# Optimization experiments

Hardware: AMD Instinct MI355X
Metric: run time of the kernel (lower is better)

## Reference

```python
import jax, jax.numpy as jnp
import numpy as np

B, T, C, H = 8, 1024, 768, 12
HD = C // H  # 64

def setup_inputs() -> dict:
    key = jax.random.key(0)
    ks = jax.random.split(key, 5)
    s = 0.02
    return {
        "x": jax.random.normal(ks[0], (B, T, C), dtype=jnp.float32),
        "w_attn": jax.random.normal(ks[1], (C, 3 * C), dtype=jnp.float32) * s,
        "b_attn": jnp.zeros((3 * C,), dtype=jnp.float32),
        "w_proj": jax.random.normal(ks[2], (C, C), dtype=jnp.float32) * s,
        "b_proj": jnp.zeros((C,), dtype=jnp.float32),
    }

def reference(x, w_attn, b_attn, w_proj, b_proj):
    Bx, Tx, Cx = x.shape
    qkv = x @ w_attn + b_attn                      # [B,T,3C]
    q, k, v = jnp.split(qkv, 3, axis=-1)
    # [B,H,T,hd]
    q = q.reshape(Bx, Tx, H, HD).transpose(0, 2, 1, 3)
    k = k.reshape(Bx, Tx, H, HD).transpose(0, 2, 1, 3)
    v = v.reshape(Bx, Tx, H, HD).transpose(0, 2, 1, 3)
    scale = 1.0 / jnp.sqrt(jnp.asarray(HD, dtype=x.dtype))
    scores = jnp.einsum('bhqd,bhkd->bhqk', q, k) * scale  # [B,H,T,T]
    causal = jnp.tril(jnp.ones((Tx, Tx), dtype=bool))
    scores = jnp.where(causal, scores, jnp.asarray(-jnp.inf, dtype=x.dtype))
    weights = jax.nn.softmax(scores, axis=-1)
    y = jnp.einsum('bhqk,bhkd->bhqd', weights, v)  # [B,H,T,hd]
    y = y.transpose(0, 2, 1, 3).reshape(Bx, Tx, Cx)
    return y @ w_proj + b_proj
```

## Files before the change

### kernel.cpp

```cpp
#include <hip/hip_runtime.h>
#include <cstdint>
#include <cstddef>

#define B_  8
#define T_  1024
#define C_  768
#define H_  12
#define HD_ 64
#define K3_ 2304

typedef unsigned short u16;
typedef __attribute__((ext_vector_type(8))) short bf16x8;
typedef __attribute__((ext_vector_type(4))) float f32x4;

#define MFMA __builtin_amdgcn_mfma_f32_16x16x32_bf16

__device__ __forceinline__ u16 f2bf(float f) {
    unsigned u = __builtin_bit_cast(unsigned, f);
    u += 0x7fffu + ((u >> 16) & 1u);
    return (u16)(u >> 16);
}

__device__ __forceinline__ unsigned pk2bf(float a, float b) {
    unsigned ua = __builtin_bit_cast(unsigned, a) + 0x8000u;
    unsigned ub = __builtin_bit_cast(unsigned, b) + 0x8000u;
    return (ua >> 16) | (ub & 0xffff0000u);
}

#define GLL16(gp, lp) __builtin_amdgcn_global_load_lds( \
    (__attribute__((address_space(1))) unsigned int*)(gp), \
    (__attribute__((address_space(3))) unsigned int*)(lp), 16, 0, 0)

__device__ __forceinline__ void tcvt_tile(const float* __restrict__ in, u16* __restrict__ out,
                                          int R, int Cc, int bx, int by, int tid, float* tile ) {
    int bc = bx * 32, br = by * 32;
    int tx = tid & 31, ty = tid >> 5;
    #pragma unroll
    for (int kk = 0; kk < 32; kk += 8)
        tile[(ty + kk) * 33 + tx] = in[(size_t)(br + ty + kk) * Cc + bc + tx];
    __syncthreads();
    #pragma unroll
    for (int kk = 0; kk < 32; kk += 8)
        out[(size_t)(bc + ty + kk) * R + br + tx] = f2bf(tile[tx * 33 + ty + kk]);
}

__global__ void prep(const float* __restrict__ x, u16* __restrict__ xb,
                     const float* __restrict__ wa, u16* __restrict__ wat,
                     const float* __restrict__ wp, u16* __restrict__ wpt) {
    __shared__ float tile[32 * 33];
    int bid = blockIdx.x, tid = threadIdx.x;
    if (bid < 6144) {
        int i = bid * 256 + tid;
        float4 v = ((const float4*)x)[i];
        ushort4 o;
        o.x = f2bf(v.x); o.y = f2bf(v.y); o.z = f2bf(v.z); o.w = f2bf(v.w);
        ((ushort4*)xb)[i] = o;
    } else if (bid < 6144 + 1728) {
        int b = bid - 6144;
        tcvt_tile(wa, wat, C_, K3_, b % 72, b / 72, tid, tile);
    } else {
        int b = bid - 7872;
        tcvt_tile(wp, wpt, C_, C_, b % 24, b / 24, tid, tile);
    }
}

#define VMW5 asm volatile("s_waitcnt vmcnt(5)" ::: "memory")
#define VMW0 asm volatile("s_waitcnt vmcnt(0)" ::: "memory")
#define BAR  __builtin_amdgcn_s_barrier()

__device__ __forceinline__ void gemm_pipe(const u16* __restrict__ A, const u16* __restrict__ Bt,
                                          int m0, int n0, u16* SM, f32x4 (&acc)[4][3]) {
    const int K = C_;
    int tid = threadIdx.x;
    int lane = tid & 63, wv = tid >> 6;
    int wr = wv >> 2, wc = wv & 3;
    int r16 = lane & 15, quad = lane >> 4;
    int sw = r16 & 7;
    int x0 = (quad ^ sw) * 8;
    int x1 = ((4 + quad) ^ sw) * 8;
    int arow = (wr * 64 + r16) * 64;
    int brow = (wc * 48 + r16) * 64;
    int tr = tid >> 3;
    int tb = (tid & 7) ^ (tr & 7);
    const u16* Ag = A  + (size_t)(m0 + tr) * K + tb * 8;
    const u16* Bg = Bt + (size_t)(n0 + tr) * K + tb * 8;
    u16* SLa = SM + tid * 8;
    u16* SLb = SM + 24576 + tid * 8;
    const u16* SMB = SM + 24576;

#define STG_T(ss, kO) { \
    GLL16(Ag + (kO),                       SLa + (ss) * 8192); \
    GLL16(Ag + (size_t)64 * K + (kO),      SLa + (ss) * 8192 + 4096); \
    GLL16(Bg + (kO),                       SLb + (ss) * 12288); \
    GLL16(Bg + (size_t)64 * K + (kO),      SLb + (ss) * 12288 + 4096); \
    GLL16(Bg + (size_t)128 * K + (kO),     SLb + (ss) * 12288 + 8192); }
#define RDH(rs, XC, af, bf) { \
    const u16* Ar_ = SM  + (rs) * 8192  + arow; \
    const u16* Br_ = SMB + (rs) * 12288 + brow; \
    _Pragma("unroll") for (int i_ = 0; i_ < 4; i_++) af[i_] = *(const bf16x8*)&Ar_[i_ * 1024 + (XC)]; \
    _Pragma("unroll") for (int j_ = 0; j_ < 3; j_++) bf[j_] = *(const bf16x8*)&Br_[j_ * 1024 + (XC)]; }
#define MMH(af, bf) { \
    __builtin_amdgcn_s_setprio(1); \
    _Pragma("unroll") for (int i_ = 0; i_ < 4; i_++) \
    _Pragma("unroll") for (int j_ = 0; j_ < 3; j_++) \
        acc[i_][j_] = MFMA(af[i_], bf[j_], acc[i_][j_], 0, 0, 0); \
    __builtin_amdgcn_s_setprio(0); }
#define PHASE(rs, ts, kO) { \
    bf16x8 a0[4], b0[3], a1[4], b1[3]; \
    RDH(rs, x0, a0, b0); RDH(rs, x1, a1, b1); \
    STG_T(ts, kO); \
    MMH(a0, b0); MMH(a1, b1); \
    VMW5; BAR; }

    STG_T(0, 0); STG_T(1, 64);
    VMW5; BAR;

    int kS = 128;
    #pragma unroll
    for (int o = 0; o < 3; ++o) {
        PHASE(0, 2, kS);
        PHASE(1, 0, kS + 64);
        PHASE(2, 1, kS + 128);
        kS += 192;
    }
    PHASE(0, 2, 704);
    {
        bf16x8 a0[4], b0[3], a1[4], b1[3];
        RDH(1, x0, a0, b0); RDH(1, x1, a1, b1);
        MMH(a0, b0); MMH(a1, b1);
        VMW0; BAR;
    }
    {
        bf16x8 a0[4], b0[3], a1[4], b1[3];
        RDH(2, x0, a0, b0); RDH(2, x1, a1, b1);
        MMH(a0, b0); MMH(a1, b1);
    }
#undef STG_T
#undef RDH
#undef MMH
#undef PHASE
}

__launch_bounds__(512)
__global__ void gemm_qkv(const u16* __restrict__ A, const u16* __restrict__ Bt,
                         const float* __restrict__ bias,
                         u16* __restrict__ q, u16* __restrict__ k, u16* __restrict__ v) {
    __shared__ __align__(16) u16 SM[61440];
    int id = blockIdx.x;
    int xcd = id & 7, j = id >> 3;
    int m0 = (xcd * 8 + (j & 7)) * 128;
    int np = j >> 3;
    f32x4 acc[4][3] = {};
    gemm_pipe(A, Bt, m0, np * 192, SM, acc);

    int tid = threadIdx.x;
    int lane = tid & 63, wv = tid >> 6;
    int wr = wv >> 2, wc = wv & 3;
    int r16 = lane & 15, quad = lane >> 4;
    __syncthreads();

    int sec = np >> 2;
    int cc0 = (np & 3) * 192;
    int b = m0 >> 10, t0 = m0 & 1023;

    if (sec == 2) {
        #pragma unroll
        for (int i = 0; i < 4; i++) {
            #pragma unroll
            for (int jj = 0; jj < 3; jj++) {
                int cc = cc0 + wc * 48 + jj * 16 + r16;
                float bv = bias[2 * C_ + cc];
                int h = cc >> 6, hd = cc & 63;
                int t = t0 + wr * 64 + i * 16 + quad * 4;
                ushort4 ov;
                ov.x = f2bf(acc[i][jj][0] + bv); ov.y = f2bf(acc[i][jj][1] + bv);
                ov.z = f2bf(acc[i][jj][2] + bv); ov.w = f2bf(acc[i][jj][3] + bv);
                *(ushort4*)(v + (((size_t)b * H_ + h) * HD_ + hd) * T_ + t) = ov;
            }
        }
    } else {
        float scale = (sec == 0) ? 0.125f : 1.0f;
        u16* dst = (sec == 0) ? q : k;
        u16 (*Cs)[200] = (u16(*)[200])SM;
        #pragma unroll
        for (int i = 0; i < 4; i++)
            #pragma unroll
            for (int jj = 0; jj < 3; jj++) {
                int col = wc * 48 + jj * 16 + r16;
                float bv = bias[sec * C_ + cc0 + col];
                #pragma unroll
                for (int r = 0; r < 4; r++)
                    Cs[wr * 64 + i * 16 + quad * 4 + r][col] = f2bf((acc[i][jj][r] + bv) * scale);
            }
        __syncthreads();
        int h0 = cc0 >> 6;
        int rsel = tid >> 3;
        int ch = tid & 7;
        #pragma unroll
        for (int p = 0; p < 2; p++)
            #pragma unroll
            for (int h3 = 0; h3 < 3; h3++) {
                int rl = p * 64 + rsel;
                uint4 val = *(const uint4*)&Cs[rl][h3 * 64 + ch * 8];
                *(uint4*)(dst + (((size_t)b * H_ + h0 + h3) * T_ + t0 + rl) * HD_ + ch * 8) = val;
            }
    }
}

__launch_bounds__(512)
__global__ void gemm_proj(const u16* __restrict__ A, const u16* __restrict__ Bt,
                          const float* __restrict__ bias, float* __restrict__ out) {
    __shared__ __align__(16) u16 SM[61440];
    int id = blockIdx.x;
    int xcd = id & 7, j = id >> 3;
    int m0 = (xcd * 8 + (j & 7)) * 128;
    int n0 = (j >> 3) * 192;
    f32x4 acc[4][3] = {};
    gemm_pipe(A, Bt, m0, n0, SM, acc);

    int tid = threadIdx.x;
    int lane = tid & 63, wv = tid >> 6;
    int wr = wv >> 2, wc = wv & 3;
    int r16 = lane & 15, quad = lane >> 4;
    #pragma unroll
    for (int i = 0; i < 4; i++) {
        #pragma unroll
        for (int jj = 0; jj < 3; jj++) {
            int gn = n0 + wc * 48 + jj * 16 + r16;
            float bv = bias[gn];
            #pragma unroll
            for (int r = 0; r < 4; r++) {
                int gm = m0 + wr * 64 + i * 16 + quad * 4 + r;
                out[(size_t)gm * C_ + gn] = acc[i][jj][r] + bv;
            }
        }
    }
}

__launch_bounds__(256, 2)
__global__ void attn(const u16* __restrict__ q, const u16* __restrict__ k,
                     const u16* __restrict__ v, u16* __restrict__ y) {
    __shared__ __align__(16) u16 Kb[2][64][64];
    __shared__ __align__(16) u16 Vb[2][64][64];
    __shared__ __align__(16) u16 P[4][2][16][72];
    int tid = threadIdx.x, lane = tid & 63, w = tid >> 6;
    int r16 = lane & 15, quad = lane >> 4;
    int id = blockIdx.x;
    int bh = id % 96;
    int bi = id / 96;
    int b = bh / H_, h = bh - b * H_;
    int x = bi * 4 + w;
    int t_lo = x, t_hi = 63 - x;
    int qb_lo = t_lo * 16, qb_hi = t_hi * 16;
    const u16* qh = q + (size_t)bh * T_ * HD_;
    const u16* kh = k + (size_t)bh * T_ * HD_;
    const u16* vh = v + (size_t)bh * HD_ * T_;

    bf16x8 ql0 = *(const bf16x8*)(qh + (size_t)(qb_lo + r16) * HD_ + quad * 8);
    bf16x8 ql1 = *(const bf16x8*)(qh + (size_t)(qb_lo + r16) * HD_ + 32 + quad * 8);
    bf16x8 qh0 = *(const bf16x8*)(qh + (size_t)(qb_hi + r16) * HD_ + quad * 8);
    bf16x8 qh1 = *(const bf16x8*)(qh + (size_t)(qb_hi + r16) * HD_ + 32 + quad * 8);

    f32x4 oL[4] = {}, oH[4] = {};
    float lL = 0.f, lH = 0.f;
    int qyL = qb_lo + r16, qyH = qb_hi + r16;
    int ilo_last = bi;
    int n64 = __builtin_amdgcn_readfirstlane(16 - bi);

    int srow = lane >> 3;
    int scb  = (lane & 7) ^ srow;
    const u16* kst = kh + (size_t)(w * 16 + srow) * HD_ + scb * 8;
    const u16* vst = vh + (size_t)(w * 16 + srow) * T_ + scb * 8;
    int swz = (r16 & 7);

    {
        #pragma unroll
        for (int s2 = 0; s2 < 2; s2++) {
            GLL16(kst + (size_t)(s2 * 8) * HD_, &Kb[0][w * 16 + s2 * 8][0] + lane * 8);
            GLL16(vst + (size_t)(s2 * 8) * T_,  &Vb[0][w * 16 + s2 * 8][0] + lane * 8);
        }
    }
    __syncthreads();

    for (int it = 0; it < n64; ++it) {
        int kv0 = it * 64;
        int buf = it & 1;
        bool lo_on = (it <= ilo_last);
        if (it + 1 < n64) {
            int kvn = kv0 + 64;
            #pragma unroll
            for (int s2 = 0; s2 < 2; s2++) {
                GLL16(kst + (size_t)(kvn + s2 * 8) * HD_, &Kb[buf ^ 1][w * 16 + s2 * 8][0] + lane * 8);
                GLL16(vst + (size_t)(s2 * 8) * T_ + kvn,  &Vb[buf ^ 1][w * 16 + s2 * 8][0] + lane * 8);
            }
        }
        bf16x8 kf[4][2];
        #pragma unroll
        for (int n = 0; n < 4; n++)
            #pragma unroll
            for (int c = 0; c < 2; c++)
                kf[n][c] = *(const bf16x8*)&Kb[buf][n * 16 + r16][((c * 4 + quad) ^ swz) * 8];
        f32x4 sH[4] = {};
        #pragma unroll
        for (int n = 0; n < 4; n++) {
            sH[n] = MFMA(kf[n][0], qh0, sH[n], 0, 0, 0);
            sH[n] = MFMA(kf[n][1], qh1, sH[n], 0, 0, 0);
        }
        if (it == n64 - 1) {
            #pragma unroll
            for (int n = 0; n < 4; n++)
                #pragma unroll
                for (int r = 0; r < 4; r++)
                    if (kv0 + n * 16 + quad * 4 + r > qyH) sH[n][r] = -1e30f;
        }
        #pragma unroll
        for (int n = 0; n < 4; n++) {
            float p0 = __expf(sH[n][0]);
            float p1 = __expf(sH[n][1]);
            float p2 = __expf(sH[n][2]);
            float p3 = __expf(sH[n][3]);
            lH += (p0 + p1) + (p2 + p3);
            uint2 pd; pd.x = pk2bf(p0, p1); pd.y = pk2bf(p2, p3);
            *(uint2*)&P[w][1][r16][n * 16 + quad * 4] = pd;
        }
        if (lo_on) {
            f32x4 sL[4] = {};
            #pragma unroll
            for (int n = 0; n < 4; n++) {
                sL[n] = MFMA(kf[n][0], ql0, sL[n], 0, 0, 0);
                sL[n] = MFMA(kf[n][1], ql1, sL[n], 0, 0, 0);
            }
            if (it == ilo_last) {
                #pragma unroll
                for (int n = 0; n < 4; n++)
                    #pragma unroll
                    for (int r = 0; r < 4; r++)
                        if (kv0 + n * 16 + quad * 4 + r > qyL) sL[n][r] = -1e30f;
            }
            #pragma unroll
            for (int n = 0; n < 4; n++) {
                float p0 = __expf(sL[n][0]);
                float p1 = __expf(sL[n][1]);
                float p2 = __expf(sL[n][2]);
                float p3 = __expf(sL[n][3]);
                lL += (p0 + p1) + (p2 + p3);
                uint2 pd; pd.x = pk2bf(p0, p1); pd.y = pk2bf(p2, p3);
                *(uint2*)&P[w][0][r16][n * 16 + quad * 4] = pd;
            }
        }
        bf16x8 vf[4][2];
        #pragma unroll
        for (int j = 0; j < 4; j++)
            #pragma unroll
            for (int c = 0; c < 2; c++)
                vf[j][c] = *(const bf16x8*)&Vb[buf][j * 16 + r16][((c * 4 + quad) ^ swz) * 8];
        #pragma unroll
        for (int c = 0; c < 2; c++) {
            bf16x8 pfH = *(const bf16x8*)&P[w][1][r16][c * 32 + quad * 8];
            #pragma unroll
            for (int j = 0; j < 4; j++)
                oH[j] = MFMA(vf[j][c], pfH, oH[j], 0, 0, 0);
        }
        if (lo_on) {
            #pragma unroll
            for (int c = 0; c < 2; c++) {
                bf16x8 pfL = *(const bf16x8*)&P[w][0][r16][c * 32 + quad * 8];
                #pragma unroll
                for (int j = 0; j < 4; j++)
                    oL[j] = MFMA(vf[j][c], pfL, oL[j], 0, 0, 0);
            }
        }
        __syncthreads();
    }

    lH += __shfl_xor(lH, 16, 64);
    lH += __shfl_xor(lH, 32, 64);
    lL += __shfl_xor(lL, 16, 64);
    lL += __shfl_xor(lL, 32, 64);
    float invH = 1.f / lH, invL = 1.f / lL;
    int tqH = qb_hi + r16, tqL = qb_lo + r16;
    #pragma unroll
    for (int j = 0; j < 4; j++) {
        ushort4 ovH, ovL;
        ovH.x = f2bf(oH[j][0] * invH); ovH.y = f2bf(oH[j][1] * invH);
        ovH.z = f2bf(oH[j][2] * invH); ovH.w = f2bf(oH[j][3] * invH);
        ovL.x = f2bf(oL[j][0] * invL); ovL.y = f2bf(oL[j][1] * invL);
        ovL.z = f2bf(oL[j][2] * invL); ovL.w = f2bf(oL[j][3] * invL);
        *(ushort4*)(y + ((size_t)b * T_ + tqH) * C_ + h * 64 + j * 16 + quad * 4) = ovH;
        *(ushort4*)(y + ((size_t)b * T_ + tqL) * C_ + h * 64 + j * 16 + quad * 4) = ovL;
    }
}

extern "C" void kernel_launch(void* const* d_in, const int* in_sizes, int n_in,
                              void* d_out, int out_size, void* d_ws, size_t ws_size,
                              hipStream_t stream) {
    const float* x      = (const float*)d_in[0];
    const float* w_attn = (const float*)d_in[1];
    const float* b_attn = (const float*)d_in[2];
    const float* w_proj = (const float*)d_in[3];
    const float* b_proj = (const float*)d_in[4];
    float* out = (float*)d_out;

    char* ws = (char*)d_ws;
    size_t off = 0;
    auto alloc = [&](size_t bytes) {
        void* p = ws + off;
        off += (bytes + 255) & ~(size_t)255;
        return p;
    };
    const size_t M = (size_t)B_ * T_;
    u16* x_bf = (u16*)alloc(M * C_ * 2);
    u16* wat  = (u16*)alloc((size_t)K3_ * C_ * 2);
    u16* wpt  = (u16*)alloc((size_t)C_ * C_ * 2);
    u16* qb   = (u16*)alloc((size_t)B_ * H_ * T_ * HD_ * 2);
    u16* kb   = (u16*)alloc((size_t)B_ * H_ * T_ * HD_ * 2);
    u16* vb   = (u16*)alloc((size_t)B_ * H_ * T_ * HD_ * 2);
    u16* yb   = (u16*)alloc(M * C_ * 2);

    prep<<<6144 + 1728 + 576, 256, 0, stream>>>(x, x_bf, w_attn, wat, w_proj, wpt);
    gemm_qkv<<<768, 512, 0, stream>>>(x_bf, wat, b_attn, qb, kb, vb);
    attn<<<8 * 96, 256, 0, stream>>>(qb, kb, vb, yb);
    gemm_proj<<<256, 512, 0, stream>>>(yb, wpt, b_proj, out);
}
```

Baseline: 159.2 us.

## Shrink GEMM tiles to 128x96 with 4 waves and double-buffered LDS

Both projection GEMMs change from 512-thread blocks computing 128x192 tiles with a triple-buffered LDS pipeline to 256-thread blocks computing 128x96 tiles with a double-buffered pipeline, which halves LDS use and allows two blocks per CU. The goal is more resident blocks and better load balance across CUs (twice as many blocks). The trade-off is a shallower prefetch with two barriers per k-step and more redundant A-tile loads across the N blocks. The q/k epilogue writes are remapped to match the narrower tile.

Result: no change. 159.1 us (-0.1%).

```diff
diff --git a/kernel.cpp b/kernel.cpp
--- a/kernel.cpp
+++ b/kernel.cpp
@@ -64,7 +64,7 @@
     }
 }
 
-#define VMW5 asm volatile("s_waitcnt vmcnt(5)" ::: "memory")
+#define VMW7 asm volatile("s_waitcnt vmcnt(7)" ::: "memory")
 #define VMW0 asm volatile("s_waitcnt vmcnt(0)" ::: "memory")
 #define BAR  __builtin_amdgcn_s_barrier()
 
@@ -73,7 +73,7 @@
     const int K = C_;
     int tid = threadIdx.x;
     int lane = tid & 63, wv = tid >> 6;
-    int wr = wv >> 2, wc = wv & 3;
+    int wr = wv >> 1, wc = wv & 1;
     int r16 = lane & 15, quad = lane >> 4;
     int sw = r16 & 7;
     int x0 = (quad ^ sw) * 8;
@@ -85,18 +85,20 @@
     const u16* Ag = A  + (size_t)(m0 + tr) * K + tb * 8;
     const u16* Bg = Bt + (size_t)(n0 + tr) * K + tb * 8;
     u16* SLa = SM + tid * 8;
-    u16* SLb = SM + 24576 + tid * 8;
-    const u16* SMB = SM + 24576;
+    u16* SLb = SM + 16384 + tid * 8;
+    const u16* SMB = SM + 16384;
 
 #define STG_T(ss, kO) { \
     GLL16(Ag + (kO),                       SLa + (ss) * 8192); \
+    GLL16(Ag + (size_t)32 * K + (kO),      SLa + (ss) * 8192 + 2048); \
     GLL16(Ag + (size_t)64 * K + (kO),      SLa + (ss) * 8192 + 4096); \
-    GLL16(Bg + (kO),                       SLb + (ss) * 12288); \
-    GLL16(Bg + (size_t)64 * K + (kO),      SLb + (ss) * 12288 + 4096); \
-    GLL16(Bg + (size_t)128 * K + (kO),     SLb + (ss) * 12288 + 8192); }
+    GLL16(Ag + (size_t)96 * K + (kO),      SLa + (ss) * 8192 + 6144); \
+    GLL16(Bg + (kO),                       SLb + (ss) * 6144); \
+    GLL16(Bg + (size_t)32 * K + (kO),      SLb + (ss) * 6144 + 2048); \
+    GLL16(Bg + (size_t)64 * K + (kO),      SLb + (ss) * 6144 + 4096); }
 #define RDH(rs, XC, af, bf) { \
-    const u16* Ar_ = SM  + (rs) * 8192  + arow; \
-    const u16* Br_ = SMB + (rs) * 12288 + brow; \
+    const u16* Ar_ = SM  + (rs) * 8192 + arow; \
+    const u16* Br_ = SMB + (rs) * 6144 + brow; \
     _Pragma("unroll") for (int i_ = 0; i_ < 4; i_++) af[i_] = *(const bf16x8*)&Ar_[i_ * 1024 + (XC)]; \
     _Pragma("unroll") for (int j_ = 0; j_ < 3; j_++) bf[j_] = *(const bf16x8*)&Br_[j_ * 1024 + (XC)]; }
 #define MMH(af, bf) { \
@@ -105,62 +107,57 @@
     _Pragma("unroll") for (int j_ = 0; j_ < 3; j_++) \
         acc[i_][j_] = MFMA(af[i_], bf[j_], acc[i_][j_], 0, 0, 0); \
     __builtin_amdgcn_s_setprio(0); }
-#define PHASE(rs, ts, kO) { \
-    bf16x8 a0[4], b0[3], a1[4], b1[3]; \
-    RDH(rs, x0, a0, b0); RDH(rs, x1, a1, b1); \
-    STG_T(ts, kO); \
-    MMH(a0, b0); MMH(a1, b1); \
-    VMW5; BAR; }
 
     STG_T(0, 0); STG_T(1, 64);
-    VMW5; BAR;
-
-    int kS = 128;
+    VMW7; BAR;
+
     #pragma unroll
-    for (int o = 0; o < 3; ++o) {
-        PHASE(0, 2, kS);
-        PHASE(1, 0, kS + 64);
-        PHASE(2, 1, kS + 128);
-        kS += 192;
-    }
-    PHASE(0, 2, 704);
+    for (int kt = 0; kt < 10; ++kt) {
+        int p = kt & 1;
+        bf16x8 a0[4], b0[3], a1[4], b1[3];
+        RDH(p, x0, a0, b0); RDH(p, x1, a1, b1);
+        MMH(a0, b0); MMH(a1, b1);
+        BAR;
+        STG_T(p, (kt + 2) * 64);
+        VMW7;
+        BAR;
+    }
+    {
+        bf16x8 a0[4], b0[3], a1[4], b1[3];
+        RDH(0, x0, a0, b0); RDH(0, x1, a1, b1);
+        MMH(a0, b0); MMH(a1, b1);
+        VMW0; BAR;
+    }
     {
         bf16x8 a0[4], b0[3], a1[4], b1[3];
         RDH(1, x0, a0, b0); RDH(1, x1, a1, b1);
         MMH(a0, b0); MMH(a1, b1);
-        VMW0; BAR;
-    }
-    {
-        bf16x8 a0[4], b0[3], a1[4], b1[3];
-        RDH(2, x0, a0, b0); RDH(2, x1, a1, b1);
-        MMH(a0, b0); MMH(a1, b1);
     }
 #undef STG_T
 #undef RDH
 #undef MMH
-#undef PHASE
-}
-
-__launch_bounds__(512)
+}
+
+__launch_bounds__(256, 2)
 __global__ void gemm_qkv(const u16* __restrict__ A, const u16* __restrict__ Bt,
                          const float* __restrict__ bias,
                          u16* __restrict__ q, u16* __restrict__ k, u16* __restrict__ v) {
-    __shared__ __align__(16) u16 SM[61440];
+    __shared__ __align__(16) u16 SM[28672];
     int id = blockIdx.x;
     int xcd = id & 7, j = id >> 3;
     int m0 = (xcd * 8 + (j & 7)) * 128;
     int np = j >> 3;
     f32x4 acc[4][3] = {};
-    gemm_pipe(A, Bt, m0, np * 192, SM, acc);
+    gemm_pipe(A, Bt, m0, np * 96, SM, acc);
 
     int tid = threadIdx.x;
     int lane = tid & 63, wv = tid >> 6;
-    int wr = wv >> 2, wc = wv & 3;
+    int wr = wv >> 1, wc = wv & 1;
     int r16 = lane & 15, quad = lane >> 4;
     __syncthreads();
 
-    int sec = np >> 2;
-    int cc0 = (np & 3) * 192;
+    int sec = np >> 3;
+    int cc0 = (np & 7) * 96;
     int b = m0 >> 10, t0 = m0 & 1023;
 
     if (sec == 2) {
@@ -181,7 +178,7 @@
     } else {
         float scale = (sec == 0) ? 0.125f : 1.0f;
         u16* dst = (sec == 0) ? q : k;
-        u16 (*Cs)[200] = (u16(*)[200])SM;
+        u16 (*Cs)[104] = (u16(*)[104])SM;
         #pragma unroll
         for (int i = 0; i < 4; i++)
             #pragma unroll
@@ -193,34 +190,35 @@
                     Cs[wr * 64 + i * 16 + quad * 4 + r][col] = f2bf((acc[i][jj][r] + bv) * scale);
             }
         __syncthreads();
-        int h0 = cc0 >> 6;
-        int rsel = tid >> 3;
-        int ch = tid & 7;
-        #pragma unroll
-        for (int p = 0; p < 2; p++)
-            #pragma unroll
-            for (int h3 = 0; h3 < 3; h3++) {
-                int rl = p * 64 + rsel;
-                uint4 val = *(const uint4*)&Cs[rl][h3 * 64 + ch * 8];
-                *(uint4*)(dst + (((size_t)b * H_ + h0 + h3) * T_ + t0 + rl) * HD_ + ch * 8) = val;
-            }
-    }
-}
-
-__launch_bounds__(512)
+        if (tid < 192) {
+            int ch = tid % 12;
+            int rsel = tid / 12;
+            int cc = cc0 + ch * 8;
+            int h = cc >> 6, hd = cc & 63;
+            u16* dbase = dst + ((size_t)b * H_ + h) * T_ * HD_ + hd;
+            #pragma unroll
+            for (int p = 0; p < 8; p++) {
+                int rl = p * 16 + rsel;
+                *(uint4*)(dbase + (size_t)(t0 + rl) * HD_) = *(const uint4*)&Cs[rl][ch * 8];
+            }
+        }
+    }
+}
+
+__launch_bounds__(256, 2)
 __global__ void gemm_proj(const u16* __restrict__ A, const u16* __restrict__ Bt,
                           const float* __restrict__ bias, float* __restrict__ out) {
-    __shared__ __align__(16) u16 SM[61440];
+    __shared__ __align__(16) u16 SM[28672];
     int id = blockIdx.x;
     int xcd = id & 7, j = id >> 3;
     int m0 = (xcd * 8 + (j & 7)) * 128;
-    int n0 = (j >> 3) * 192;
+    int n0 = (j >> 3) * 96;
     f32x4 acc[4][3] = {};
     gemm_pipe(A, Bt, m0, n0, SM, acc);
 
     int tid = threadIdx.x;
     int lane = tid & 63, wv = tid >> 6;
-    int wr = wv >> 2, wc = wv & 3;
+    int wr = wv >> 1, wc = wv & 1;
     int r16 = lane & 15, quad = lane >> 4;
     #pragma unroll
     for (int i = 0; i < 4; i++) {
@@ -418,7 +416,7 @@
     u16* yb   = (u16*)alloc(M * C_ * 2);
 
     prep<<<6144 + 1728 + 576, 256, 0, stream>>>(x, x_bf, w_attn, wat, w_proj, wpt);
-    gemm_qkv<<<768, 512, 0, stream>>>(x_bf, wat, b_attn, qb, kb, vb);
+    gemm_qkv<<<1536, 256, 0, stream>>>(x_bf, wat, b_attn, qb, kb, vb);
     attn<<<8 * 96, 256, 0, stream>>>(qb, kb, vb, yb);
-    gemm_proj<<<256, 512, 0, stream>>>(yb, wpt, b_proj, out);
-}
+    gemm_proj<<<512, 256, 0, stream>>>(yb, wpt, b_proj, out);
+}
```
